# Kernel optimization log

Hardware: AMD Instinct MI355X
Metric: run time of the kernel (lower is better)

## Reference

```python
import jax, jax.numpy as jnp
import numpy as np

N, D, E = 32768, 768, 8
F = 4 * D  # 3072


def setup_inputs() -> dict:
    key = jax.random.key(0)
    ks = jax.random.split(key, 8)
    scale = 0.02
    hidden_states = jax.random.normal(ks[0], (N, D), dtype=jnp.float32)
    Wg = jax.random.normal(ks[1], (E, D), dtype=jnp.float32) * scale  # gate, no bias
    W1 = jax.random.normal(ks[2], (E, F, D), dtype=jnp.float32) * scale
    b1 = jnp.zeros((E, F), dtype=jnp.float32)
    W2 = jax.random.normal(ks[3], (E, D, F), dtype=jnp.float32) * scale
    b2 = jnp.zeros((E, D), dtype=jnp.float32)
    W3 = jax.random.normal(ks[4], (E, 1, D), dtype=jnp.float32) * scale
    b3 = jnp.zeros((E, 1), dtype=jnp.float32)
    return {"hidden_states": hidden_states, "Wg": Wg, "W1": W1, "b1": b1,
            "W2": W2, "b2": b2, "W3": W3, "b3": b3, "top_k": 2}


def reference(hidden_states, Wg, W1, b1, W2, b2, W3, b3, top_k):
    x = hidden_states  # [N, D]
    logits = x @ Wg.T  # [N, E]
    probs = jax.nn.softmax(logits.astype(jnp.float32), axis=-1)
    w, _sel = jax.lax.top_k(probs, top_k)  # [N, k] (descending)
    w = (w / w.sum(axis=-1, keepdims=True)).astype(x.dtype)
    # FAITHFUL TO SOURCE BUG: expert used is the position index j (experts[j]),
    # not the selected expert id. So densely run experts 0..top_k-1 on all tokens.
    W1k, b1k = W1[:top_k], b1[:top_k]
    W2k, b2k = W2[:top_k], b2[:top_k]
    W3k, b3k = W3[:top_k], b3[:top_k]
    # dropout is identity in eval mode
    h = jax.nn.relu(jnp.einsum('nd,kfd->knf', x, W1k) + b1k[:, None, :])  # [k,N,F]
    o = x[None, :, :] + jnp.einsum('knf,kdf->knd', h, W2k) + b2k[:, None, :]  # residual, [k,N,D]
    s = jnp.einsum('knd,kod->kno', o, W3k) + b3k[:, None, :]  # [k,N,1]
    out = jnp.sum(jnp.swapaxes(w, 0, 1)[:, :, None] * s, axis=0)  # [N,1]
    return out
```

## Files before the change

### kernel.cpp

```cpp
#include <hip/hip_runtime.h>
#include <hip/hip_bf16.h>
#include <stdint.h>

#define N_TOK 32768
#define DDIM  768
#define FDIM  3072
#define NCOLS (2*FDIM)
#define BK    64
#define KTILES (DDIM/BK)
#define NTILES (NCOLS/256)
#define VD_CHUNK 96

typedef __attribute__((ext_vector_type(8))) short bf16x8;
typedef __attribute__((ext_vector_type(4))) float f32x4;

__device__ __forceinline__ unsigned short f2bf(float f) {
  unsigned u = __builtin_bit_cast(unsigned, f);
  unsigned r = (u + 0x7fffu + ((u >> 16) & 1u)) >> 16;
  return (unsigned short)r;
}

__device__ __forceinline__ void gl_lds16(const void* g, void* l) {
  __builtin_amdgcn_global_load_lds(
      (const __attribute__((address_space(1))) unsigned int*)g,
      (__attribute__((address_space(3))) unsigned int*)l, 16, 0, 0);
}

__global__ __launch_bounds__(256) void cvt_kernel(const float* __restrict__ src,
                                                  unsigned short* __restrict__ dst) {
  size_t i = ((size_t)blockIdx.x * 256 + threadIdx.x) * 4;
  float4 f = *(const float4*)(src + i);
  ushort4 u;
  u.x = f2bf(f.x); u.y = f2bf(f.y); u.z = f2bf(f.z); u.w = f2bf(f.w);
  *(ushort4*)(dst + i) = u;
}

__global__ __launch_bounds__(256) void vcalc_kernel(const float* __restrict__ W2,
                                                    const float* __restrict__ W3,
                                                    float* __restrict__ vpart) {
  __shared__ float w3s[VD_CHUNK];
  int k  = blockIdx.x / 12;
  int fb = blockIdx.x % 12;
  int db = blockIdx.y;
  if (threadIdx.x < VD_CHUNK) w3s[threadIdx.x] = W3[k*DDIM + db*VD_CHUNK + threadIdx.x];
  __syncthreads();
  int f = fb*256 + threadIdx.x;
  const float* W2k = W2 + (size_t)k*DDIM*FDIM + (size_t)db*VD_CHUNK*FDIM + f;
  float s = 0.f;
  #pragma unroll 8
  for (int d = 0; d < VD_CHUNK; ++d) s += W2k[(size_t)d*FDIM] * w3s[d];
  vpart[(size_t)db*NCOLS + k*FDIM + f] = s;
}

__global__ __launch_bounds__(256) void vfinal_kernel(const float* __restrict__ vpart,
                                                     float* __restrict__ v,
                                                     const float* __restrict__ b2,
                                                     const float* __restrict__ W3,
                                                     const float* __restrict__ b3,
                                                     float* __restrict__ cbuf) {
  int f = blockIdx.x*256 + threadIdx.x;
  float s = 0.f;
  #pragma unroll
  for (int db = 0; db < 8; ++db) s += vpart[(size_t)db*NCOLS + f];
  v[f] = s;
  if (blockIdx.x == 0 && threadIdx.x < 128) {
    int k = threadIdx.x >> 6, lane = threadIdx.x & 63;
    float c = 0.f;
    #pragma unroll
    for (int it = 0; it < DDIM/64; ++it) {
      int i = it*64 + lane;
      c += b2[k*DDIM + i] * W3[k*DDIM + i];
    }
    #pragma unroll
    for (int m = 1; m < 64; m <<= 1) c += __shfl_xor(c, m, 64);
    if (lane == 0) cbuf[k] = c + b3[k];
  }
}

__global__ __launch_bounds__(256) void gate_cvt_kernel(
    const float* __restrict__ x, const float* __restrict__ Wg,
    const float* __restrict__ W3, const float* __restrict__ cbuf,
    unsigned short* __restrict__ xbf,
    float* __restrict__ wgt, float* __restrict__ base) {
  int wid  = threadIdx.x >> 6;
  int lane = threadIdx.x & 63;
  int n = blockIdx.x * 4 + wid;
  const float4* xr = (const float4*)(x + (size_t)n * DDIM);
  ushort4* xw = (ushort4*)(xbf + (size_t)n * DDIM);
  float acc[8] = {0,0,0,0,0,0,0,0};
  float d30 = 0.f, d31 = 0.f;
  #pragma unroll
  for (int it = 0; it < DDIM/256; ++it) {
    int i = it*64 + lane;
    float4 xv = xr[i];
    ushort4 u;
    u.x = f2bf(xv.x); u.y = f2bf(xv.y); u.z = f2bf(xv.z); u.w = f2bf(xv.w);
    xw[i] = u;
    #pragma unroll
    for (int e = 0; e < 8; ++e) {
      float4 w = ((const float4*)(Wg + e*DDIM))[i];
      acc[e] += xv.x*w.x + xv.y*w.y + xv.z*w.z + xv.w*w.w;
    }
    float4 wa = ((const float4*)W3)[i];
    d30 += xv.x*wa.x + xv.y*wa.y + xv.z*wa.z + xv.w*wa.w;
    float4 wb = ((const float4*)(W3 + DDIM))[i];
    d31 += xv.x*wb.x + xv.y*wb.y + xv.z*wb.z + xv.w*wb.w;
  }
  #pragma unroll
  for (int m = 1; m < 64; m <<= 1) {
    #pragma unroll
    for (int e = 0; e < 8; ++e) acc[e] += __shfl_xor(acc[e], m, 64);
    d30 += __shfl_xor(d30, m, 64);
    d31 += __shfl_xor(d31, m, 64);
  }
  if (lane == 0) {
    float l1 = acc[0]; int a1 = 0;
    #pragma unroll
    for (int e = 1; e < 8; ++e) if (acc[e] > l1) { l1 = acc[e]; a1 = e; }
    float l2 = -3.4e38f;
    #pragma unroll
    for (int e = 0; e < 8; ++e) if (e != a1 && acc[e] > l2) l2 = acc[e];
    float w0 = 1.f / (1.f + __expf(l2 - l1));
    float w1 = 1.f - w0;
    wgt[2*n]   = w0;
    wgt[2*n+1] = w1;
    base[n] = w0 * (d30 + cbuf[0]) + w1 * (d31 + cbuf[1]);
  }
}

__global__ __launch_bounds__(512, 2) void gemm_kernel(
    const unsigned short* __restrict__ A,
    const unsigned short* __restrict__ B,
    const float* __restrict__ b1,
    const float* __restrict__ v,
    float* __restrict__ part) {
  __shared__ __align__(16) char smem[131072];

  const int tid  = threadIdx.x;
  const int lane = tid & 63, wid = tid >> 6;
  const int wm = wid >> 2, wn = wid & 3;
  const int q  = lane >> 4, cl = lane & 15;

  const int b  = blockIdx.x;
  const int L  = (b & 7) * 384 + (b >> 3);
  const int bn = L % 24;
  const int bm = L / 24;

  const unsigned short* Ab = A + (size_t)bm * 256 * DDIM;
  const unsigned short* Bb = B + (size_t)bn * 256 * DDIM;

  const size_t srow = (size_t)(wid*16 + cl) * DDIM + q*8;

  const int lb = lane * 16;
  const int aBase = wm*8192 + lb;
  const int bBase = 16384 + wn*4096 + lb;

  f32x4 zero = {0.f, 0.f, 0.f, 0.f};
  f32x4 acc[8][4];
  #pragma unroll
  for (int i = 0; i < 8; ++i)
    #pragma unroll
    for (int j = 0; j < 4; ++j) acc[i][j] = zero;

  auto stageA = [&](int t, int ks) {
    char* dst = smem + (t & 1) * 65536 + ks * 32768;
    const unsigned short* s0 = Ab + srow + t*BK + ks*32;
    gl_lds16(s0,            dst + wid*1024);
    gl_lds16(s0 + 128*DDIM, dst + 8192 + wid*1024);
  };
  auto stageB = [&](int t, int ks) {
    char* dst = smem + (t & 1) * 65536 + ks * 32768 + 16384;
    const unsigned short* s0 = Bb + srow + t*BK + ks*32;
    gl_lds16(s0,            dst + wid*1024);
    gl_lds16(s0 + 128*DDIM, dst + 8192 + wid*1024);
  };

  stageA(0, 0); stageB(0, 0);
  stageA(0, 1); stageB(0, 1);
  stageA(1, 0); stageB(1, 0);
  asm volatile("s_waitcnt vmcnt(8)" ::: "memory");
  __builtin_amdgcn_s_barrier();
  __builtin_amdgcn_sched_barrier(0);

  #pragma unroll
  for (int kt = 0; kt < KTILES; ++kt) {
    const char* ct = smem + (kt & 1) * 65536;
    bf16x8 a0[4], a1[4], bf0[4];

    #pragma unroll
    for (int n = 0; n < 4; ++n) bf0[n] = *(const bf16x8*)(ct + bBase + n*1024);
    #pragma unroll
    for (int m = 0; m < 4; ++m) a0[m] = *(const bf16x8*)(ct + aBase + m*1024);
    #pragma unroll
    for (int m = 0; m < 4; ++m) a1[m] = *(const bf16x8*)(ct + aBase + 4096 + m*1024);
    if (kt <= 10) { stageA(kt + 1, 1); stageB(kt + 1, 1); }
    __builtin_amdgcn_s_setprio(1);
    #pragma unroll
    for (int m = 0; m < 4; ++m)
      #pragma unroll
      for (int n = 0; n < 4; ++n)
        acc[m][n] = __builtin_amdgcn_mfma_f32_16x16x32_bf16(a0[m], bf0[n], acc[m][n], 0, 0, 0);
    #pragma unroll
    for (int m = 0; m < 4; ++m)
      #pragma unroll
      for (int n = 0; n < 4; ++n)
        acc[4 + m][n] = __builtin_amdgcn_mfma_f32_16x16x32_bf16(a1[m], bf0[n], acc[4 + m][n], 0, 0, 0);
    __builtin_amdgcn_s_setprio(0);
    if (kt <= 10) { asm volatile("s_waitcnt vmcnt(8)" ::: "memory"); }
    else          { asm volatile("s_waitcnt vmcnt(0)" ::: "memory"); }
    __builtin_amdgcn_s_barrier();
    __builtin_amdgcn_sched_barrier(0);

    #pragma unroll
    for (int n = 0; n < 4; ++n) bf0[n] = *(const bf16x8*)(ct + 32768 + bBase + n*1024);
    #pragma unroll
    for (int m = 0; m < 4; ++m) a0[m] = *(const bf16x8*)(ct + 32768 + aBase + m*1024);
    #pragma unroll
    for (int m = 0; m < 4; ++m) a1[m] = *(const bf16x8*)(ct + 32768 + aBase + 4096 + m*1024);
    if (kt <= 9) { stageA(kt + 2, 0); stageB(kt + 2, 0); }
    __builtin_amdgcn_s_setprio(1);
    #pragma unroll
    for (int m = 0; m < 4; ++m)
      #pragma unroll
      for (int n = 0; n < 4; ++n)
        acc[m][n] = __builtin_amdgcn_mfma_f32_16x16x32_bf16(a0[m], bf0[n], acc[m][n], 0, 0, 0);
    #pragma unroll
    for (int m = 0; m < 4; ++m)
      #pragma unroll
      for (int n = 0; n < 4; ++n)
        acc[4 + m][n] = __builtin_amdgcn_mfma_f32_16x16x32_bf16(a1[m], bf0[n], acc[4 + m][n], 0, 0, 0);
    __builtin_amdgcn_s_setprio(0);
    if (kt <= 9)       { asm volatile("s_waitcnt vmcnt(8)" ::: "memory"); }
    else if (kt == 10) { asm volatile("s_waitcnt vmcnt(4)" ::: "memory"); }
    __builtin_amdgcn_s_barrier();
    __builtin_amdgcn_sched_barrier(0);
  }

  float vv[4], bb[4];
  #pragma unroll
  for (int n = 0; n < 4; ++n) {
    int cg = bn*256 + wn*64 + n*16 + cl;
    vv[n] = v[cg];
    bb[n] = b1[cg];
  }
  float* red = (float*)smem;
  #pragma unroll
  for (int mt = 0; mt < 8; ++mt) {
    #pragma unroll
    for (int rr = 0; rr < 4; ++rr) {
      float s = 0.f;
      #pragma unroll
      for (int n = 0; n < 4; ++n) {
        float val = acc[mt][n][rr] + bb[n];
        s += fmaxf(val, 0.f) * vv[n];
      }
      #pragma unroll
      for (int msk = 1; msk < 16; msk <<= 1) s += __shfl_xor(s, msk, 64);
      if (cl == 0) red[(wm*128 + mt*16 + q*4 + rr)*4 + wn] = s;
    }
  }
  __syncthreads();
  if (tid < 256) {
    float r4 = red[tid*4] + red[tid*4+1] + red[tid*4+2] + red[tid*4+3];
    part[(size_t)bn * N_TOK + (size_t)bm*256 + tid] = r4;
  }
}

__global__ __launch_bounds__(256) void final_kernel(const float* __restrict__ part,
                                                    const float* __restrict__ wgt,
                                                    const float* __restrict__ base,
                                                    float* __restrict__ out) {
  int n = blockIdx.x * 256 + threadIdx.x;
  float s0 = 0.f, s1 = 0.f;
  #pragma unroll
  for (int t = 0; t < 12; ++t) s0 += part[(size_t)t*N_TOK + n];
  #pragma unroll
  for (int t = 12; t < 24; ++t) s1 += part[(size_t)t*N_TOK + n];
  out[n] = base[n] + wgt[2*n]*s0 + wgt[2*n+1]*s1;
}

extern "C" void kernel_launch(void* const* d_in, const int* in_sizes, int n_in,
                              void* d_out, int out_size, void* d_ws, size_t ws_size,
                              hipStream_t stream) {
  const float* x  = (const float*)d_in[0];
  const float* Wg = (const float*)d_in[1];
  const float* W1 = (const float*)d_in[2];
  const float* b1 = (const float*)d_in[3];
  const float* W2 = (const float*)d_in[4];
  const float* b2 = (const float*)d_in[5];
  const float* W3 = (const float*)d_in[6];
  const float* b3 = (const float*)d_in[7];
  float* out = (float*)d_out;

  char* ws = (char*)d_ws;
  size_t off = 0;
  auto alloc = [&](size_t bytes) -> char* {
    char* p = ws + off;
    off += (bytes + 255) & ~(size_t)255;
    return p;
  };
  unsigned short* xbf  = (unsigned short*)alloc((size_t)N_TOK * DDIM * 2);
  unsigned short* w1bf = (unsigned short*)alloc((size_t)NCOLS * DDIM * 2);
  float* vpart = (float*)alloc((size_t)8 * NCOLS * 4);
  float* v     = (float*)alloc((size_t)NCOLS * 4);
  float* cbuf  = (float*)alloc(64);
  float* wgt   = (float*)alloc((size_t)N_TOK * 2 * 4);
  float* base  = (float*)alloc((size_t)N_TOK * 4);
  float* part  = (float*)alloc((size_t)NTILES * N_TOK * 4);
  if (off > ws_size) return;

  cvt_kernel<<<(NCOLS*DDIM)/1024, 256, 0, stream>>>(W1, w1bf);
  vcalc_kernel<<<dim3(24, 8), 256, 0, stream>>>(W2, W3, vpart);
  vfinal_kernel<<<NCOLS/256, 256, 0, stream>>>(vpart, v, b2, W3, b3, cbuf);
  gate_cvt_kernel<<<N_TOK/4, 256, 0, stream>>>(x, Wg, W3, cbuf, xbf, wgt, base);
  gemm_kernel<<<3072, 512, 0, stream>>>(xbf, w1bf, b1, v, part);
  final_kernel<<<N_TOK/256, 256, 0, stream>>>(part, wgt, base, out);
}
```

Baseline: 626.6 us.

## Shrink GEMM tile to 256x128 with 256 threads, triple-buffered BK=32 pipeline

The fused GEMM block shrinks from 256x256 with 8 waves to 256x128 with 4 waves. The K loop now uses a 3-stage LDS ring with BK=32 instead of a double buffer of 64-wide K tiles, and the XCD-aware block remapping is replaced by a plain 2D grid. Partial sums from each pair of column tiles are combined with atomicAdd into 24 part slices, which requires a memset first. This cuts LDS use per block and may raise occupancy, at the cost of more A-tile reloads, atomic traffic, and losing the L2-friendly block ordering.

```diff
diff --git a/kernel.cpp b/kernel.cpp
--- a/kernel.cpp
+++ b/kernel.cpp
@@ -6,9 +6,10 @@
 #define DDIM  768
 #define FDIM  3072
 #define NCOLS (2*FDIM)
-#define BK    64
-#define KTILES (DDIM/BK)
-#define NTILES (NCOLS/256)
+#define BK    32
+#define KSTEPS (DDIM/BK)
+#define NTILES (NCOLS/128)
+#define PARTS  24
 #define VD_CHUNK 96
 
 typedef __attribute__((ext_vector_type(8))) short bf16x8;
@@ -128,32 +129,27 @@
   }
 }
 
-__global__ __launch_bounds__(512, 2) void gemm_kernel(
+__global__ __launch_bounds__(256, 2) void gemm_kernel(
     const unsigned short* __restrict__ A,
     const unsigned short* __restrict__ B,
     const float* __restrict__ b1,
     const float* __restrict__ v,
     float* __restrict__ part) {
-  __shared__ __align__(16) char smem[131072];
+  __shared__ __align__(16) char smem[73728];
 
   const int tid  = threadIdx.x;
   const int lane = tid & 63, wid = tid >> 6;
-  const int wm = wid >> 2, wn = wid & 3;
+  const int wm = wid >> 1, wn = wid & 1;
   const int q  = lane >> 4, cl = lane & 15;
-
-  const int b  = blockIdx.x;
-  const int L  = (b & 7) * 384 + (b >> 3);
-  const int bn = L % 24;
-  const int bm = L / 24;
+  const int bn = blockIdx.x;
+  const int bm = blockIdx.y;
 
   const unsigned short* Ab = A + (size_t)bm * 256 * DDIM;
-  const unsigned short* Bb = B + (size_t)bn * 256 * DDIM;
+  const unsigned short* Bb = B + (size_t)bn * 128 * DDIM;
 
   const size_t srow = (size_t)(wid*16 + cl) * DDIM + q*8;
 
   const int lb = lane * 16;
-  const int aBase = wm*8192 + lb;
-  const int bBase = 16384 + wn*4096 + lb;
 
   f32x4 zero = {0.f, 0.f, 0.f, 0.f};
   f32x4 acc[8][4];
@@ -162,107 +158,73 @@
     #pragma unroll
     for (int j = 0; j < 4; ++j) acc[i][j] = zero;
 
-  auto stageA = [&](int t, int ks) {
-    char* dst = smem + (t & 1) * 65536 + ks * 32768;
-    const unsigned short* s0 = Ab + srow + t*BK + ks*32;
-    gl_lds16(s0,            dst + wid*1024);
-    gl_lds16(s0 + 128*DDIM, dst + 8192 + wid*1024);
+  auto stage = [&](int u) {
+    char* d = smem + (u % 3) * 24576;
+    const unsigned short* sA = Ab + srow + u * BK;
+    #pragma unroll
+    for (int j = 0; j < 4; ++j)
+      gl_lds16(sA + (size_t)j * 64 * DDIM, d + (j*4 + wid) * 1024);
+    const unsigned short* sB = Bb + srow + u * BK;
+    #pragma unroll
+    for (int j = 0; j < 2; ++j)
+      gl_lds16(sB + (size_t)j * 64 * DDIM, d + 16384 + (j*4 + wid) * 1024);
   };
-  auto stageB = [&](int t, int ks) {
-    char* dst = smem + (t & 1) * 65536 + ks * 32768 + 16384;
-    const unsigned short* s0 = Bb + srow + t*BK + ks*32;
-    gl_lds16(s0,            dst + wid*1024);
-    gl_lds16(s0 + 128*DDIM, dst + 8192 + wid*1024);
-  };
-
-  stageA(0, 0); stageB(0, 0);
-  stageA(0, 1); stageB(0, 1);
-  stageA(1, 0); stageB(1, 0);
-  asm volatile("s_waitcnt vmcnt(8)" ::: "memory");
+
+  stage(0);
+  stage(1);
+  asm volatile("s_waitcnt vmcnt(6)" ::: "memory");
   __builtin_amdgcn_s_barrier();
   __builtin_amdgcn_sched_barrier(0);
 
   #pragma unroll
-  for (int kt = 0; kt < KTILES; ++kt) {
-    const char* ct = smem + (kt & 1) * 65536;
-    bf16x8 a0[4], a1[4], bf0[4];
-
-    #pragma unroll
-    for (int n = 0; n < 4; ++n) bf0[n] = *(const bf16x8*)(ct + bBase + n*1024);
-    #pragma unroll
-    for (int m = 0; m < 4; ++m) a0[m] = *(const bf16x8*)(ct + aBase + m*1024);
-    #pragma unroll
-    for (int m = 0; m < 4; ++m) a1[m] = *(const bf16x8*)(ct + aBase + 4096 + m*1024);
-    if (kt <= 10) { stageA(kt + 1, 1); stageB(kt + 1, 1); }
+  for (int t = 0; t < KSTEPS; ++t) {
+    const char* cb = smem + (t % 3) * 24576;
+    bf16x8 af[8], bf[4];
+    #pragma unroll
+    for (int n = 0; n < 4; ++n) bf[n] = *(const bf16x8*)(cb + 16384 + (wn*4 + n)*1024 + lb);
+    #pragma unroll
+    for (int m = 0; m < 8; ++m) af[m] = *(const bf16x8*)(cb + (wm*8 + m)*1024 + lb);
+    if (t <= KSTEPS - 3) stage(t + 2);
     __builtin_amdgcn_s_setprio(1);
     #pragma unroll
-    for (int m = 0; m < 4; ++m)
+    for (int m = 0; m < 8; ++m)
       #pragma unroll
       for (int n = 0; n < 4; ++n)
-        acc[m][n] = __builtin_amdgcn_mfma_f32_16x16x32_bf16(a0[m], bf0[n], acc[m][n], 0, 0, 0);
-    #pragma unroll
-    for (int m = 0; m < 4; ++m)
-      #pragma unroll
-      for (int n = 0; n < 4; ++n)
-        acc[4 + m][n] = __builtin_amdgcn_mfma_f32_16x16x32_bf16(a1[m], bf0[n], acc[4 + m][n], 0, 0, 0);
+        acc[m][n] = __builtin_amdgcn_mfma_f32_16x16x32_bf16(af[m], bf[n], acc[m][n], 0, 0, 0);
     __builtin_amdgcn_s_setprio(0);
-    if (kt <= 10) { asm volatile("s_waitcnt vmcnt(8)" ::: "memory"); }
-    else          { asm volatile("s_waitcnt vmcnt(0)" ::: "memory"); }
+    if (t <= KSTEPS - 3)      { asm volatile("s_waitcnt vmcnt(6)" ::: "memory"); }
+    else if (t == KSTEPS - 2) { asm volatile("s_waitcnt vmcnt(0)" ::: "memory"); }
     __builtin_amdgcn_s_barrier();
     __builtin_amdgcn_sched_barrier(0);
-
-    #pragma unroll
-    for (int n = 0; n < 4; ++n) bf0[n] = *(const bf16x8*)(ct + 32768 + bBase + n*1024);
-    #pragma unroll
-    for (int m = 0; m < 4; ++m) a0[m] = *(const bf16x8*)(ct + 32768 + aBase + m*1024);
-    #pragma unroll
-    for (int m = 0; m < 4; ++m) a1[m] = *(const bf16x8*)(ct + 32768 + aBase + 4096 + m*1024);
-    if (kt <= 9) { stageA(kt + 2, 0); stageB(kt + 2, 0); }
-    __builtin_amdgcn_s_setprio(1);
-    #pragma unroll
-    for (int m = 0; m < 4; ++m)
-      #pragma unroll
-      for (int n = 0; n < 4; ++n)
-        acc[m][n] = __builtin_amdgcn_mfma_f32_16x16x32_bf16(a0[m], bf0[n], acc[m][n], 0, 0, 0);
-    #pragma unroll
-    for (int m = 0; m < 4; ++m)
-      #pragma unroll
-      for (int n = 0; n < 4; ++n)
-        acc[4 + m][n] = __builtin_amdgcn_mfma_f32_16x16x32_bf16(a1[m], bf0[n], acc[4 + m][n], 0, 0, 0);
-    __builtin_amdgcn_s_setprio(0);
-    if (kt <= 9)       { asm volatile("s_waitcnt vmcnt(8)" ::: "memory"); }
-    else if (kt == 10) { asm volatile("s_waitcnt vmcnt(4)" ::: "memory"); }
-    __builtin_amdgcn_s_barrier();
-    __builtin_amdgcn_sched_barrier(0);
-  }
-
-  float vv[4], bb[4];
+  }
+
+  float vv[4], bb1[4];
   #pragma unroll
   for (int n = 0; n < 4; ++n) {
-    int cg = bn*256 + wn*64 + n*16 + cl;
+    int cg = bn*128 + wn*64 + n*16 + cl;
     vv[n] = v[cg];
-    bb[n] = b1[cg];
+    bb1[n] = b1[cg];
   }
   float* red = (float*)smem;
   #pragma unroll
-  for (int mt = 0; mt < 8; ++mt) {
+  for (int m = 0; m < 8; ++m) {
     #pragma unroll
     for (int rr = 0; rr < 4; ++rr) {
       float s = 0.f;
       #pragma unroll
       for (int n = 0; n < 4; ++n) {
-        float val = acc[mt][n][rr] + bb[n];
+        float val = acc[m][n][rr] + bb1[n];
         s += fmaxf(val, 0.f) * vv[n];
       }
       #pragma unroll
       for (int msk = 1; msk < 16; msk <<= 1) s += __shfl_xor(s, msk, 64);
-      if (cl == 0) red[(wm*128 + mt*16 + q*4 + rr)*4 + wn] = s;
+      if (cl == 0) red[(wm*128 + m*16 + q*4 + rr)*2 + wn] = s;
     }
   }
   __syncthreads();
   if (tid < 256) {
-    float r4 = red[tid*4] + red[tid*4+1] + red[tid*4+2] + red[tid*4+3];
-    part[(size_t)bn * N_TOK + (size_t)bm*256 + tid] = r4;
+    float r = red[tid*2] + red[tid*2+1];
+    atomicAdd(&part[(size_t)(bn >> 1) * N_TOK + (size_t)bm*256 + tid], r);
   }
 }
 
@@ -306,13 +268,14 @@
   float* cbuf  = (float*)alloc(64);
   float* wgt   = (float*)alloc((size_t)N_TOK * 2 * 4);
   float* base  = (float*)alloc((size_t)N_TOK * 4);
-  float* part  = (float*)alloc((size_t)NTILES * N_TOK * 4);
+  float* part  = (float*)alloc((size_t)PARTS * N_TOK * 4);
   if (off > ws_size) return;
 
   cvt_kernel<<<(NCOLS*DDIM)/1024, 256, 0, stream>>>(W1, w1bf);
   vcalc_kernel<<<dim3(24, 8), 256, 0, stream>>>(W2, W3, vpart);
   vfinal_kernel<<<NCOLS/256, 256, 0, stream>>>(vpart, v, b2, W3, b3, cbuf);
   gate_cvt_kernel<<<N_TOK/4, 256, 0, stream>>>(x, Wg, W3, cbuf, xbf, wgt, base);
-  gemm_kernel<<<3072, 512, 0, stream>>>(xbf, w1bf, b1, v, part);
+  hipMemsetAsync(part, 0, (size_t)PARTS * N_TOK * 4, stream);
+  gemm_kernel<<<dim3(NTILES, N_TOK/256), 256, 0, stream>>>(xbf, w1bf, b1, v, part);
   final_kernel<<<N_TOK/256, 256, 0, stream>>>(part, wgt, base, out);
 }
```

Measured after the change: 659.1 us. +5.2%, slower.
